# Performance work log

Hardware: AMD Instinct MI355X
Metric: run time of the kernel (lower is better)

The kernel has to match this reference:

```python
import jax, jax.numpy as jnp
import numpy as np

B, C, H, W = 64, 2048, 14, 14
D, S, ITERS, EPS, HID = 256, 8, 3, 1e-8, 512


def build_pos(h, w, d):
    gy, gx = np.meshgrid(np.arange(h), np.arange(w), indexing='ij')
    q = d // 4
    omega = 1.0 / (10000.0 ** (np.arange(q) / q))
    ey = gy.reshape(-1, 1) * omega
    ex = gx.reshape(-1, 1) * omega
    pe = np.concatenate([np.sin(ey), np.cos(ey), np.sin(ex), np.cos(ex)], axis=1)
    return jnp.asarray(pe[None], jnp.float32)  # (1, h*w, d)


def layernorm(x, g, b, eps=1e-5):
    m = x.mean(-1, keepdims=True)
    v = ((x - m) ** 2).mean(-1, keepdims=True)
    return (x - m) * jax.lax.rsqrt(v + eps) * g + b


def setup_inputs() -> dict:
    key = jax.random.key(0)
    ks = jax.random.split(key, 16)
    w = lambda k, shp, s=0.02: jax.random.normal(k, shp, jnp.float32) * s
    inp = {
        'x': jax.random.normal(ks[0], (B, C, H, W), jnp.float32),
        'slot_noise': jax.random.normal(ks[1], (B, S, D), jnp.float32),
        'conv_w': w(ks[2], (C, D)), 'conv_b': jnp.zeros((D,), jnp.float32),
        'pos': build_pos(H, W, D),
        'slots_mu': jax.random.normal(ks[3], (1, 1, D), jnp.float32),
        'slots_logsigma': -jnp.ones((1, 1, D), jnp.float32),
        'qw': w(ks[4], (D, D)), 'qb': jnp.zeros((D,), jnp.float32),
        'kw': w(ks[5], (D, D)), 'kb': jnp.zeros((D,), jnp.float32),
        'vw': w(ks[6], (D, D)), 'vb': jnp.zeros((D,), jnp.float32),
        'gru_wih': w(ks[7], (D, 3 * D)), 'gru_whh': w(ks[8], (D, 3 * D)),
        'gru_bih': jnp.zeros((3 * D,), jnp.float32), 'gru_bhh': jnp.zeros((3 * D,), jnp.float32),
        'w1': w(ks[9], (D, HID)), 'b1': jnp.zeros((HID,), jnp.float32),
        'w2': w(ks[10], (HID, D)), 'b2': jnp.zeros((D,), jnp.float32),
        'ln_in_g': jnp.ones((D,), jnp.float32), 'ln_in_b': jnp.zeros((D,), jnp.float32),
        'ln_s_g': jnp.ones((D,), jnp.float32), 'ln_s_b': jnp.zeros((D,), jnp.float32),
        'ln_ff_g': jnp.ones((D,), jnp.float32), 'ln_ff_b': jnp.zeros((D,), jnp.float32),
    }
    return inp


def reference(x, slot_noise, conv_w, conv_b, pos, slots_mu, slots_logsigma,
              qw, qb, kw, kb, vw, vb, gru_wih, gru_whh, gru_bih, gru_bhh,
              w1, b1, w2, b2, ln_in_g, ln_in_b, ln_s_g, ln_s_b, ln_ff_g, ln_ff_b):
    b, c, h, w_ = x.shape
    d = qw.shape[0]
    scale = d ** (-0.5)
    # (B,C,H,W) -> (B,N,C) -> project -> add pos
    xt = x.transpose(0, 2, 3, 1).reshape(b, h * w_, c)
    xt = xt @ conv_w + conv_b + pos
    # slot init
    slots = slots_mu + jnp.exp(slots_logsigma) * slot_noise  # (B,S,D)
    inp = layernorm(xt, ln_in_g, ln_in_b)
    k = inp @ kw + kb
    v = inp @ vw + vb
    attn = None
    for _ in range(ITERS):
        slots_prev = slots
        s = layernorm(slots, ln_s_g, ln_s_b)
        q = s @ qw + qb
        dots = jnp.einsum('bid,bjd->bij', q, k) * scale  # (B,S,N)
        attn = jax.nn.softmax(dots, axis=1) + EPS  # softmax over slots
        attn = attn / attn.sum(-1, keepdims=True)  # renormalize over keys
        updates = jnp.einsum('bjd,bij->bid', v, attn)  # (B,S,D)
        # GRUCell (torch semantics)
        gi = updates @ gru_wih + gru_bih
        gh = slots_prev @ gru_whh + gru_bhh
        ir, iz, inn = jnp.split(gi, 3, axis=-1)
        hr, hz, hn = jnp.split(gh, 3, axis=-1)
        r = jax.nn.sigmoid(ir + hr)
        z = jax.nn.sigmoid(iz + hz)
        nn_ = jnp.tanh(inn + r * hn)
        slots = (1.0 - z) * nn_ + z * slots_prev
        ff = layernorm(slots, ln_ff_g, ln_ff_b)
        slots = slots + (jax.nn.relu(ff @ w1 + b1)) @ w2 + b2
    attn_map = attn.reshape(b, S, h, w_)
    return slots, attn_map
```

## Files before the change

### kernel.cpp

```cpp
#include <hip/hip_runtime.h>
#include <stdint.h>

#define HWN 196
#define CIN 2048
#define DD  256
#define BB  64
#define NSLOT 8
#define KVPAD 224
#define MTOT 12544
#define BKP 128

typedef __attribute__((ext_vector_type(8))) short short8;
typedef __attribute__((ext_vector_type(4))) float f32x4;
typedef __attribute__((ext_vector_type(4))) unsigned short us4;

__device__ __forceinline__ ushort f2bf(float f){ union{float f;uint32_t u;}v;v.f=f;uint32_t u=v.u;return (ushort)((u+0x7FFFu+((u>>16)&1u))>>16);}
__device__ __forceinline__ float bf2f(ushort h){ union{uint32_t u;float f;}v;v.u=((uint32_t)h)<<16;return v.f;}
__device__ __forceinline__ float sigm(float x){ return 1.f/(1.f+expf(-x)); }

__device__ __forceinline__ short8 ldsY(const ushort* buf, int LD, int kt, int lane){
    int row = lane & 15;
    int ch = kt*4 + (lane>>4);
    return *(const short8*)&buf[row*LD + ((ch ^ (row&7))<<3)];
}
__device__ __forceinline__ short8 gX(const ushort* base, int K, int nrow, int kt, int lane){
    return *(const short8*)&base[(size_t)nrow*K + kt*32 + (lane>>4)*8];
}

struct TD { const float* s; ushort* d; int R, C, t0; };
struct TD8 { TD a[8]; };

__global__ __launch_bounds__(256) void k_prep(TD8 td){
    __shared__ float tile[32][33];
    int bt = blockIdx.x;
    int mi = 0;
    #pragma unroll
    for (int i = 1; i < 8; ++i) if (bt >= td.a[i].t0) mi = i;
    TD d = td.a[mi];
    int lt = bt - d.t0;
    int tilesx = (d.C + 31) >> 5;
    int cb = (lt % tilesx) * 32, rb = (lt / tilesx) * 32;
    int tx = threadIdx.x & 31, ty = threadIdx.x >> 5;
    for (int i = ty; i < 32; i += 8) {
        int r = rb + i, c = cb + tx;
        tile[i][tx] = (r < d.R && c < d.C) ? d.s[(size_t)r * d.C + c] : 0.f;
    }
    __syncthreads();
    for (int i = ty; i < 32; i += 8) {
        int c = cb + i, r = rb + tx;
        if (c < d.C && r < d.R) d.d[(size_t)c * d.R + r] = f2bf(tile[tx][i]);
    }
}

__global__ __launch_bounds__(512) void k_proj(const float* __restrict__ x,
        const ushort* __restrict__ cwT, float* __restrict__ Cpart){
    __shared__ ushort As[2][64*BKP];
    const int t = threadIdx.x, lane = t & 63, wv = t >> 6;
    const int tile = blockIdx.x >> 1, kq = blockIdx.x & 1;
    const int bm = tile * 64;
    const int kbase = kq * 1024;

    const int am = t & 63, kg = t >> 6;
    const int mg = bm + am;
    const int ab = mg / HWN, ap = mg % HWN;
    const float* aptr = x + (size_t)ab*(CIN*HWN) + ap + (size_t)kbase*HWN;

    f32x4 acc[4][2] = {};
    float areg[16];

    #pragma unroll
    for (int j = 0; j < 16; ++j) areg[j] = aptr[(size_t)(kg*16+j)*HWN];
    {
        short8 av0, av1;
        #pragma unroll
        for (int j = 0; j < 8; ++j){ av0[j] = (short)f2bf(areg[j]); av1[j] = (short)f2bf(areg[8+j]); }
        int ch0 = kg*2;
        *(short8*)&As[0][am*BKP + ((ch0^(am&7))<<3)] = av0;
        *(short8*)&As[0][am*BKP + (((ch0+1)^(am&7))<<3)] = av1;
    }
    __syncthreads();
    int cur = 0;
    for (int kt = 0; kt < 8; ++kt){
        if (kt < 7){
            #pragma unroll
            for (int j = 0; j < 16; ++j)
                areg[j] = aptr[(size_t)((kt+1)*BKP + kg*16+j)*HWN];
        }
        short8 bfr[4][2];
        #pragma unroll
        for (int kk = 0; kk < 4; ++kk)
            #pragma unroll
            for (int ni = 0; ni < 2; ++ni){
                int n = wv*32 + ni*16 + (lane&15);
                bfr[kk][ni] = *(const short8*)&cwT[(size_t)n*CIN + kbase + kt*BKP + kk*32 + (lane>>4)*8];
            }
        #pragma unroll
        for (int kk = 0; kk < 4; ++kk){
            short8 afr[4];
            #pragma unroll
            for (int mi = 0; mi < 4; ++mi){
                int row = mi*16 + (lane&15);
                int ch = kk*4 + (lane>>4);
                afr[mi] = *(const short8*)&As[cur][row*BKP + ((ch^(row&7))<<3)];
            }
            #pragma unroll
            for (int mi = 0; mi < 4; ++mi)
                #pragma unroll
                for (int ni = 0; ni < 2; ++ni)
                    acc[mi][ni] = __builtin_amdgcn_mfma_f32_16x16x32_bf16(afr[mi], bfr[kk][ni], acc[mi][ni], 0,0,0);
        }
        if (kt < 7){
            short8 av0, av1;
            #pragma unroll
            for (int j = 0; j < 8; ++j){ av0[j] = (short)f2bf(areg[j]); av1[j] = (short)f2bf(areg[8+j]); }
            int ch0 = kg*2;
            *(short8*)&As[cur^1][am*BKP + ((ch0^(am&7))<<3)] = av0;
            *(short8*)&As[cur^1][am*BKP + (((ch0+1)^(am&7))<<3)] = av1;
        }
        __syncthreads();
        cur ^= 1;
    }
    float* outp = Cpart + (size_t)kq*MTOT*DD;
    #pragma unroll
    for (int mi = 0; mi < 4; ++mi){
        #pragma unroll
        for (int ni = 0; ni < 2; ++ni){
            int n = wv*32 + ni*16 + (lane&15);
            #pragma unroll
            for (int r = 0; r < 4; ++r){
                int m = bm + mi*16 + (lane>>4)*4 + r;
                outp[(size_t)m*DD + n] = acc[mi][ni][r];
            }
        }
    }
}

__global__ __launch_bounds__(512) void k_red(const float* __restrict__ Cpart,
        const float* __restrict__ cb, const float* __restrict__ pos,
        const float* __restrict__ lng, const float* __restrict__ lnb,
        const ushort* __restrict__ kwT, const ushort* __restrict__ vwT,
        const float* __restrict__ kb, const float* __restrict__ vb,
        ushort* __restrict__ kbf, ushort* __restrict__ vT){
    __shared__ ushort As[32*256];
    const int t = threadIdx.x, lane = t & 63, wv = t >> 6;
    const int b = blockIdx.x / 7, pblk = blockIdx.x % 7;
    {
        int row = t >> 4, seg = t & 15;
        int pin = pblk*32 + row;
        int grow = b*HWN + pin;
        if (grow > MTOT-1) grow = MTOT-1;
        int p = pin < HWN ? pin : HWN-1;
        const float* c0 = Cpart + (size_t)grow*DD + seg*16;
        const float* c1 = Cpart + (size_t)MTOT*DD + (size_t)grow*DD + seg*16;
        const float* pp = pos + (size_t)p*DD + seg*16;
        float f[16];
        float s = 0.f, sq = 0.f;
        #pragma unroll
        for (int q = 0; q < 4; ++q){
            f32x4 a  = *(const f32x4*)&c0[q*4];
            f32x4 bq = *(const f32x4*)&c1[q*4];
            f32x4 pv = *(const f32x4*)&pp[q*4];
            f32x4 cv = *(const f32x4*)&cb[seg*16 + q*4];
            #pragma unroll
            for (int r2 = 0; r2 < 4; ++r2){
                float v = a[r2] + bq[r2] + pv[r2] + cv[r2];
                f[q*4+r2] = v; s += v; sq += v*v;
            }
        }
        #pragma unroll
        for (int m = 8; m >= 1; m >>= 1){ s += __shfl_xor(s, m, 64); sq += __shfl_xor(sq, m, 64); }
        float mean = s * (1.f/256.f);
        float rs = rsqrtf(sq*(1.f/256.f) - mean*mean + 1e-5f);
        int d0 = seg*16;
        short8 o0, o1;
        #pragma unroll
        for (int j = 0; j < 8; ++j){
            o0[j] = (short)f2bf((f[j]   - mean)*rs*lng[d0+j]   + lnb[d0+j]);
            o1[j] = (short)f2bf((f[8+j] - mean)*rs*lng[d0+8+j] + lnb[d0+8+j]);
        }
        int ch0 = seg*2;
        *(short8*)&As[row*256 + ((ch0^(row&7))<<3)] = o0;
        *(short8*)&As[row*256 + (((ch0+1)^(row&7))<<3)] = o1;
    }
    __syncthreads();
    f32x4 acck[2][2] = {}, accv[2][2] = {};
    const int n0 = wv*32;
    #pragma unroll
    for (int kt = 0; kt < 8; ++kt){
        short8 afr[2];
        #pragma unroll
        for (int mi = 0; mi < 2; ++mi){
            int row = mi*16 + (lane&15);
            int ch = kt*4 + (lane>>4);
            afr[mi] = *(const short8*)&As[row*256 + ((ch^(row&7))<<3)];
        }
        #pragma unroll
        for (int ni = 0; ni < 2; ++ni){
            int n = n0 + ni*16 + (lane&15);
            int koff = kt*32 + (lane>>4)*8;
            short8 bk = *(const short8*)&kwT[(size_t)n*DD + koff];
            short8 bv = *(const short8*)&vwT[(size_t)n*DD + koff];
            #pragma unroll
            for (int mi = 0; mi < 2; ++mi){
                acck[mi][ni] = __builtin_amdgcn_mfma_f32_16x16x32_bf16(afr[mi], bk, acck[mi][ni],0,0,0);
                accv[mi][ni] = __builtin_amdgcn_mfma_f32_16x16x32_bf16(afr[mi], bv, accv[mi][ni],0,0,0);
            }
        }
    }
    #pragma unroll
    for (int mi = 0; mi < 2; ++mi){
        #pragma unroll
        for (int ni = 0; ni < 2; ++ni){
            int n = n0 + ni*16 + (lane&15);
            float kbn = kb[n], vbn = vb[n];
            int pl0 = pblk*32 + mi*16 + (lane>>4)*4;
            us4 pk;
            #pragma unroll
            for (int r = 0; r < 4; ++r){
                kbf[((size_t)b*KVPAD + pl0 + r)*DD + n] = f2bf(acck[mi][ni][r] + kbn);
                pk[r] = f2bf(accv[mi][ni][r] + vbn);
            }
            *(us4*)&vT[((size_t)b*DD + n)*KVPAD + pl0] = pk;
        }
    }
}

__global__ __launch_bounds__(512) void k_init(const float* __restrict__ noise,
        const float* __restrict__ mu, const float* __restrict__ lsig,
        const ushort* __restrict__ qwT, const float* __restrict__ qb,
        const float* __restrict__ gs, const float* __restrict__ bs,
        float* __restrict__ slots, ushort* __restrict__ qbuf){
    __shared__ float Sld[16*256];
    __shared__ ushort Ysn[16*256];
    __shared__ float part[8][16][2];
    __shared__ float stats[16][2];
    const int t = threadIdx.x, lane = t & 63, w = t >> 6;
    const int bb = blockIdx.x, rbase = bb*16;
    {
        int row = t>>5, ch = t&31; int d = ch*8;
        f32x4 n0 = *(const f32x4*)&noise[(size_t)(rbase+row)*DD + d];
        f32x4 n1 = *(const f32x4*)&noise[(size_t)(rbase+row)*DD + d + 4];
        f32x4 m0 = *(const f32x4*)&mu[d];
        f32x4 m1 = *(const f32x4*)&mu[d+4];
        f32x4 l0 = *(const f32x4*)&lsig[d];
        f32x4 l1 = *(const f32x4*)&lsig[d+4];
        f32x4 s0, s1;
        #pragma unroll
        for (int j = 0; j < 4; ++j){
            s0[j] = m0[j] + expf(l0[j])*n0[j];
            s1[j] = m1[j] + expf(l1[j])*n1[j];
        }
        *(f32x4*)&slots[(size_t)(rbase+row)*DD + d] = s0;
        *(f32x4*)&slots[(size_t)(rbase+row)*DD + d + 4] = s1;
        *(f32x4*)&Sld[row*256 + d] = s0;
        *(f32x4*)&Sld[row*256 + d + 4] = s1;
    }
    __syncthreads();
    f32x4 sv[2];
    #pragma unroll
    for (int sub = 0; sub < 2; ++sub){
        int d0 = w*32 + sub*16 + (lane>>4)*4;
        sv[sub] = *(const f32x4*)&Sld[(lane&15)*256 + d0];
    }
    {
        float lsum = 0.f, lsq = 0.f;
        #pragma unroll
        for (int sub = 0; sub < 2; ++sub)
            #pragma unroll
            for (int r = 0; r < 4; ++r){ float v = sv[sub][r]; lsum += v; lsq += v*v; }
        lsum += __shfl_xor(lsum, 16, 64); lsum += __shfl_xor(lsum, 32, 64);
        lsq  += __shfl_xor(lsq, 16, 64);  lsq  += __shfl_xor(lsq, 32, 64);
        if (lane < 16){ part[w][lane][0] = lsum; part[w][lane][1] = lsq; }
    }
    __syncthreads();
    if (t < 16){
        float a = 0.f, c = 0.f;
        #pragma unroll
        for (int i = 0; i < 8; ++i){ a += part[i][t][0]; c += part[i][t][1]; }
        float mean = a*(1.f/256.f);
        stats[t][0] = mean;
        stats[t][1] = rsqrtf(c*(1.f/256.f) - mean*mean + 1e-5f);
    }
    __syncthreads();
    {
        int slot = lane&15;
        float mean = stats[slot][0], rs = stats[slot][1];
        #pragma unroll
        for (int sub = 0; sub < 2; ++sub){
            int d0 = w*32 + sub*16 + (lane>>4)*4;
            f32x4 g4 = *(const f32x4*)&gs[d0];
            f32x4 b4 = *(const f32x4*)&bs[d0];
            us4 o;
            #pragma unroll
            for (int r = 0; r < 4; ++r) o[r] = f2bf((sv[sub][r]-mean)*rs*g4[r] + b4[r]);
            int ch = d0>>3;
            *(us4*)&Ysn[slot*256 + ((ch^(slot&7))<<3) + (d0&7)] = o;
        }
    }
    __syncthreads();
    f32x4 qa[2] = {};
    #pragma unroll
    for (int kt = 0; kt < 8; ++kt){
        short8 ysn = ldsY(Ysn, 256, kt, lane);
        #pragma unroll
        for (int sub = 0; sub < 2; ++sub){
            int nrow = w*32 + sub*16 + (lane&15);
            short8 xx = gX(qwT, 256, nrow, kt, lane);
            qa[sub] = __builtin_amdgcn_mfma_f32_16x16x32_bf16(xx, ysn, qa[sub], 0,0,0);
        }
    }
    #pragma unroll
    for (int sub = 0; sub < 2; ++sub){
        int qd0 = w*32 + sub*16 + (lane>>4)*4;
        f32x4 qb4 = *(const f32x4*)&qb[qd0];
        us4 o;
        #pragma unroll
        for (int r = 0; r < 4; ++r) o[r] = f2bf((qa[sub][r]+qb4[r])*0.0625f);
        *(us4*)&qbuf[(size_t)(rbase+(lane&15))*DD + qd0] = o;
    }
}

__global__ __launch_bounds__(512) void k_slot(
        const ushort* __restrict__ qbuf, const ushort* __restrict__ kbf,
        const ushort* __restrict__ vT, float* __restrict__ slots,
        ushort* __restrict__ qout,
        const ushort* __restrict__ wihT, const ushort* __restrict__ whhT,
        const float* __restrict__ bih, const float* __restrict__ bhh,
        const ushort* __restrict__ w1T, const float* __restrict__ b1,
        const ushort* __restrict__ w2T, const float* __restrict__ b2,
        const float* __restrict__ gff, const float* __restrict__ bff,
        const float* __restrict__ gs, const float* __restrict__ bs,
        const ushort* __restrict__ qwT, const float* __restrict__ qb,
        float* __restrict__ out_slots, float* __restrict__ out_attn,
        int final_){
    __shared__ ushort Yq[16*256];
    __shared__ ushort Xat[16*256];
    __shared__ ushort Yupd[16*256];
    __shared__ ushort Yslb[16*256];
    __shared__ ushort Ysn[16*256];
    __shared__ ushort Yh[16*512];
    __shared__ float wpart[8][16];
    __shared__ float invk[16];
    __shared__ float part[8][16][2];
    __shared__ float stats[16][2];
    const int t = threadIdx.x, lane = t & 63, w = t >> 6;
    const int b = blockIdx.x;
    const int rbase = b * NSLOT;
    const int srow = lane & 15;
    const int srd = (srow < NSLOT) ? srow : 0;

    if (t < 256){
        int row = t>>5, ch = t&31;
        short8 v = *(const short8*)&qbuf[(size_t)(rbase+row)*DD + ch*8];
        *(short8*)&Yq[row*256 + ((ch^(row&7))<<3)] = v;
        f32x4 s0 = *(const f32x4*)&slots[(size_t)(rbase+row)*DD + ch*8];
        f32x4 s1 = *(const f32x4*)&slots[(size_t)(rbase+row)*DD + ch*8 + 4];
        short8 sv;
        #pragma unroll
        for (int j = 0; j < 4; ++j){ sv[j] = (short)f2bf(s0[j]); sv[4+j] = (short)f2bf(s1[j]); }
        *(short8*)&Yslb[row*256 + ((ch^(row&7))<<3)] = sv;
    } else {
        int i = t - 256;
        int row = (i>>5) + 8, ch = i&31;
        short8 z;
        #pragma unroll
        for (int j = 0; j < 8; ++j) z[j] = 0;
        *(short8*)&Yq[row*256 + ((ch^(row&7))<<3)] = z;
        *(short8*)&Yupd[row*256 + ((ch^(row&7))<<3)] = z;
        *(short8*)&Yslb[row*256 + ((ch^(row&7))<<3)] = z;
    }
    __syncthreads();
    {
        short8 yf[8];
        #pragma unroll
        for (int kt = 0; kt < 8; ++kt) yf[kt] = ldsY(Yq, 256, kt, lane);
        float ps = 0.f;
        #pragma unroll
        for (int rep = 0; rep < 2; ++rep){
            int f = w + rep*8;
            if (f < 14){
                f32x4 acc = {};
                #pragma unroll
                for (int kt = 0; kt < 8; ++kt){
                    short8 xx = gX(kbf + (size_t)b*KVPAD*DD, 256, f*16 + (lane&15), kt, lane);
                    acc = __builtin_amdgcn_mfma_f32_16x16x32_bf16(xx, yf[kt], acc, 0,0,0);
                }
                int k0 = f*16 + (lane>>4)*4;
                us4 o;
                #pragma unroll
                for (int r = 0; r < 4; ++r){
                    float v = acc[r];
                    float mx = v;
                    mx = fmaxf(mx, __shfl_xor(mx, 1, 64));
                    mx = fmaxf(mx, __shfl_xor(mx, 2, 64));
                    mx = fmaxf(mx, __shfl_xor(mx, 4, 64));
                    float e = expf(v - mx);
                    float se = e;
                    se += __shfl_xor(se, 1, 64);
                    se += __shfl_xor(se, 2, 64);
                    se += __shfl_xor(se, 4, 64);
                    float val = e/se + 1e-8f;
                    if (k0 + r >= HWN) val = 0.f;
                    ps += val;
                    o[r] = f2bf(val);
                }
                int ch = k0 >> 3;
                *(us4*)&Xat[srow*256 + ((ch^(srow&7))<<3) + (k0&7)] = o;
            }
        }
        ps += __shfl_xor(ps, 16, 64);
        ps += __shfl_xor(ps, 32, 64);
        if (lane < 16) wpart[w][lane] = ps;
    }
    __syncthreads();
    if (t < 16){
        float s = 0.f;
        #pragma unroll
        for (int i = 0; i < 8; ++i) s += wpart[i][t];
        invk[t] = 1.f/s;
    }
    __syncthreads();
    {
        short8 xa[7];
        #pragma unroll
        for (int kt = 0; kt < 7; ++kt) xa[kt] = ldsY(Xat, 256, kt, lane);
        f32x4 iv = *(const f32x4*)&invk[(lane>>4)*4];
        #pragma unroll
        for (int i = 0; i < 2; ++i){
            int d0 = (w*2 + i)*16;
            f32x4 acc = {};
            #pragma unroll
            for (int kt = 0; kt < 7; ++kt){
                short8 y = gX(vT + (size_t)b*DD*KVPAD, KVPAD, d0 + (lane&15), kt, lane);
                acc = __builtin_amdgcn_mfma_f32_16x16x32_bf16(xa[kt], y, acc, 0,0,0);
            }
            #pragma unroll
            for (int r = 0; r < 4; ++r){
                int s2 = (lane>>4)*4 + r;
                if (s2 < NSLOT){
                    int d = d0 + (lane&15);
                    int ch = d >> 3;
                    Yupd[s2*256 + ((ch^(s2&7))<<3) + (d&7)] = f2bf(acc[r]*iv[r]);
                }
            }
        }
    }
    if (final_){
        for (int idx = t; idx < NSLOT*HWN; idx += 512){
            int slot = idx/HWN, key = idx - slot*HWN;
            int ch = key >> 3;
            out_attn[(size_t)b*NSLOT*HWN + idx] =
                bf2f(Xat[slot*256 + ((ch^(slot&7))<<3) + (key&7)]) * invk[slot];
        }
    }
    __syncthreads();
    f32x4 gi[6] = {}, gh[6] = {};
    #pragma unroll
    for (int kt = 0; kt < 8; ++kt){
        short8 yu = ldsY(Yupd, 256, kt, lane);
        short8 ys = ldsY(Yslb, 256, kt, lane);
        #pragma unroll
        for (int g = 0; g < 3; ++g)
            #pragma unroll
            for (int sub = 0; sub < 2; ++sub){
                int nrow = g*256 + w*32 + sub*16 + (lane&15);
                short8 xi = gX(wihT, 256, nrow, kt, lane);
                short8 xh = gX(whhT, 256, nrow, kt, lane);
                gi[g*2+sub] = __builtin_amdgcn_mfma_f32_16x16x32_bf16(xi, yu, gi[g*2+sub], 0,0,0);
                gh[g*2+sub] = __builtin_amdgcn_mfma_f32_16x16x32_bf16(xh, ys, gh[g*2+sub], 0,0,0);
            }
    }
    f32x4 snew[2];
    #pragma unroll
    for (int sub = 0; sub < 2; ++sub){
        int d0 = w*32 + sub*16 + (lane>>4)*4;
        f32x4 sp  = *(const f32x4*)&slots[(size_t)(rbase + srd)*DD + d0];
        f32x4 bir = *(const f32x4*)&bih[d0];
        f32x4 biz = *(const f32x4*)&bih[256 + d0];
        f32x4 bin = *(const f32x4*)&bih[512 + d0];
        f32x4 bhr = *(const f32x4*)&bhh[d0];
        f32x4 bhz = *(const f32x4*)&bhh[256 + d0];
        f32x4 bhn = *(const f32x4*)&bhh[512 + d0];
        #pragma unroll
        for (int r = 0; r < 4; ++r){
            float ir = gi[0+sub][r] + bir[r];
            float iz = gi[2+sub][r] + biz[r];
            float in_ = gi[4+sub][r] + bin[r];
            float hr = gh[0+sub][r] + bhr[r];
            float hz = gh[2+sub][r] + bhz[r];
            float hn = gh[4+sub][r] + bhn[r];
            float rr = sigm(ir + hr);
            float zz = sigm(iz + hz);
            float nn = tanhf(in_ + rr*hn);
            snew[sub][r] = (1.f - zz)*nn + zz*sp[r];
        }
    }
    {
        float lsum = 0.f, lsq = 0.f;
        #pragma unroll
        for (int sub = 0; sub < 2; ++sub)
            #pragma unroll
            for (int r = 0; r < 4; ++r){ float v = snew[sub][r]; lsum += v; lsq += v*v; }
        lsum += __shfl_xor(lsum, 16, 64); lsum += __shfl_xor(lsum, 32, 64);
        lsq  += __shfl_xor(lsq, 16, 64);  lsq  += __shfl_xor(lsq, 32, 64);
        if (lane < 16){ part[w][lane][0] = lsum; part[w][lane][1] = lsq; }
    }
    __syncthreads();
    if (t < 16){
        float a = 0.f, c = 0.f;
        #pragma unroll
        for (int i = 0; i < 8; ++i){ a += part[i][t][0]; c += part[i][t][1]; }
        float mean = a*(1.f/256.f);
        stats[t][0] = mean;
        stats[t][1] = rsqrtf(c*(1.f/256.f) - mean*mean + 1e-5f);
    }
    __syncthreads();
    {
        float mean = stats[srow][0], rs = stats[srow][1];
        #pragma unroll
        for (int sub = 0; sub < 2; ++sub){
            int d0 = w*32 + sub*16 + (lane>>4)*4;
            f32x4 g4 = *(const f32x4*)&gff[d0];
            f32x4 b4 = *(const f32x4*)&bff[d0];
            us4 o;
            #pragma unroll
            for (int r = 0; r < 4; ++r) o[r] = f2bf((snew[sub][r]-mean)*rs*g4[r] + b4[r]);
            int ch = d0 >> 3;
            *(us4*)&Ysn[srow*256 + ((ch^(srow&7))<<3) + (d0&7)] = o;
        }
    }
    __syncthreads();
    {
        f32x4 hh[4] = {};
        #pragma unroll
        for (int kt = 0; kt < 8; ++kt){
            short8 ysn = ldsY(Ysn, 256, kt, lane);
            #pragma unroll
            for (int s2 = 0; s2 < 4; ++s2){
                int nrow = w*64 + s2*16 + (lane&15);
                short8 xx = gX(w1T, 256, nrow, kt, lane);
                hh[s2] = __builtin_amdgcn_mfma_f32_16x16x32_bf16(xx, ysn, hh[s2], 0,0,0);
            }
        }
        #pragma unroll
        for (int s2 = 0; s2 < 4; ++s2){
            int n0 = w*64 + s2*16 + (lane>>4)*4;
            f32x4 b14 = *(const f32x4*)&b1[n0];
            us4 o;
            #pragma unroll
            for (int r = 0; r < 4; ++r) o[r] = f2bf(fmaxf(hh[s2][r] + b14[r], 0.f));
            int ch = n0 >> 3;
            *(us4*)&Yh[srow*512 + ((ch^(srow&7))<<3) + (n0&7)] = o;
        }
    }
    __syncthreads();
    f32x4 ns[2];
    {
        f32x4 o2[2] = {};
        #pragma unroll
        for (int kt = 0; kt < 16; ++kt){
            short8 yh = ldsY(Yh, 512, kt, lane);
            #pragma unroll
            for (int sub = 0; sub < 2; ++sub){
                int nrow = w*32 + sub*16 + (lane&15);
                short8 xx = gX(w2T, 512, nrow, kt, lane);
                o2[sub] = __builtin_amdgcn_mfma_f32_16x16x32_bf16(xx, yh, o2[sub], 0,0,0);
            }
        }
        float* dst = final_ ? out_slots : slots;
        #pragma unroll
        for (int sub = 0; sub < 2; ++sub){
            int d0 = w*32 + sub*16 + (lane>>4)*4;
            f32x4 b24 = *(const f32x4*)&b2[d0];
            #pragma unroll
            for (int r = 0; r < 4; ++r) ns[sub][r] = o2[sub][r] + b24[r] + snew[sub][r];
            if (srow < NSLOT)
                *(f32x4*)&dst[(size_t)(rbase + srow)*DD + d0] = ns[sub];
        }
    }
    if (final_) return;
    {
        float lsum = 0.f, lsq = 0.f;
        #pragma unroll
        for (int sub = 0; sub < 2; ++sub)
            #pragma unroll
            for (int r = 0; r < 4; ++r){ float v = ns[sub][r]; lsum += v; lsq += v*v; }
        lsum += __shfl_xor(lsum, 16, 64); lsum += __shfl_xor(lsum, 32, 64);
        lsq  += __shfl_xor(lsq, 16, 64);  lsq  += __shfl_xor(lsq, 32, 64);
        if (lane < 16){ part[w][lane][0] = lsum; part[w][lane][1] = lsq; }
    }
    __syncthreads();
    if (t < 16){
        float a = 0.f, c = 0.f;
        #pragma unroll
        for (int i = 0; i < 8; ++i){ a += part[i][t][0]; c += part[i][t][1]; }
        float mean = a*(1.f/256.f);
        stats[t][0] = mean;
        stats[t][1] = rsqrtf(c*(1.f/256.f) - mean*mean + 1e-5f);
    }
    __syncthreads();
    {
        float mean = stats[srow][0], rs = stats[srow][1];
        #pragma unroll
        for (int sub = 0; sub < 2; ++sub){
            int d0 = w*32 + sub*16 + (lane>>4)*4;
            f32x4 g4 = *(const f32x4*)&gs[d0];
            f32x4 b4 = *(const f32x4*)&bs[d0];
            us4 o;
            #pragma unroll
            for (int r = 0; r < 4; ++r) o[r] = f2bf((ns[sub][r]-mean)*rs*g4[r] + b4[r]);
            int ch = d0 >> 3;
            *(us4*)&Ysn[srow*256 + ((ch^(srow&7))<<3) + (d0&7)] = o;
        }
    }
    __syncthreads();
    {
        f32x4 qa[2] = {};
        #pragma unroll
        for (int kt = 0; kt < 8; ++kt){
            short8 ysn = ldsY(Ysn, 256, kt, lane);
            #pragma unroll
            for (int sub = 0; sub < 2; ++sub){
                int nrow = w*32 + sub*16 + (lane&15);
                short8 xx = gX(qwT, 256, nrow, kt, lane);
                qa[sub] = __builtin_amdgcn_mfma_f32_16x16x32_bf16(xx, ysn, qa[sub], 0,0,0);
            }
        }
        #pragma unroll
        for (int sub = 0; sub < 2; ++sub){
            int qd0 = w*32 + sub*16 + (lane>>4)*4;
            f32x4 qb4 = *(const f32x4*)&qb[qd0];
            us4 o;
            #pragma unroll
            for (int r = 0; r < 4; ++r) o[r] = f2bf((qa[sub][r]+qb4[r])*0.0625f);
            if (srow < NSLOT)
                *(us4*)&qout[(size_t)(rbase + srow)*DD + qd0] = o;
        }
    }
}

extern "C" void kernel_launch(void* const* d_in, const int* in_sizes, int n_in,
                              void* d_out, int out_size, void* d_ws, size_t ws_size,
                              hipStream_t stream) {
    const float* x      = (const float*)d_in[0];
    const float* noise  = (const float*)d_in[1];
    const float* conv_w = (const float*)d_in[2];
    const float* conv_b = (const float*)d_in[3];
    const float* pos    = (const float*)d_in[4];
    const float* mu     = (const float*)d_in[5];
    const float* logsig = (const float*)d_in[6];
    const float* qw  = (const float*)d_in[7];
    const float* qb  = (const float*)d_in[8];
    const float* kw  = (const float*)d_in[9];
    const float* kb  = (const float*)d_in[10];
    const float* vw  = (const float*)d_in[11];
    const float* vb  = (const float*)d_in[12];
    const float* wih = (const float*)d_in[13];
    const float* whh = (const float*)d_in[14];
    const float* bih = (const float*)d_in[15];
    const float* bhh = (const float*)d_in[16];
    const float* w1  = (const float*)d_in[17];
    const float* b1  = (const float*)d_in[18];
    const float* w2  = (const float*)d_in[19];
    const float* b2  = (const float*)d_in[20];
    const float* g_in = (const float*)d_in[21];
    const float* b_in = (const float*)d_in[22];
    const float* g_s  = (const float*)d_in[23];
    const float* b_s  = (const float*)d_in[24];
    const float* g_ff = (const float*)d_in[25];
    const float* b_ff = (const float*)d_in[26];

    char* w = (char*)d_ws;
    ushort* kbf    = (ushort*)w; w += (size_t)BB*KVPAD*DD*2;
    ushort* vT     = (ushort*)w; w += (size_t)BB*DD*KVPAD*2;
    ushort* cwT    = (ushort*)w; w += (size_t)DD*CIN*2;
    ushort* qwT    = (ushort*)w; w += (size_t)DD*DD*2;
    ushort* kwT    = (ushort*)w; w += (size_t)DD*DD*2;
    ushort* vwT    = (ushort*)w; w += (size_t)DD*DD*2;
    ushort* wihT   = (ushort*)w; w += (size_t)768*DD*2;
    ushort* whhT   = (ushort*)w; w += (size_t)768*DD*2;
    ushort* w1T    = (ushort*)w; w += (size_t)512*DD*2;
    ushort* w2T    = (ushort*)w; w += (size_t)DD*512*2;
    ushort* qbb    = (ushort*)w; w += (size_t)BB*NSLOT*DD*2;
    float*  slotsb = (float*)w;  w += (size_t)BB*NSLOT*DD*4;
    float*  Cpart  = (float*)w;  w += (size_t)2*MTOT*DD*4;

    float* out_slots = (float*)d_out;
    float* out_attn  = (float*)d_out + (size_t)BB*NSLOT*DD;

    TD8 td;
    td.a[0] = { conv_w, cwT, 2048, 256,    0 };
    td.a[1] = { qw,     qwT,  256, 256,  512 };
    td.a[2] = { kw,     kwT,  256, 256,  576 };
    td.a[3] = { vw,     vwT,  256, 256,  640 };
    td.a[4] = { wih,    wihT, 256, 768,  704 };
    td.a[5] = { whh,    whhT, 256, 768,  896 };
    td.a[6] = { w1,     w1T,  256, 512, 1088 };
    td.a[7] = { w2,     w2T,  512, 256, 1216 };

    k_prep<<<1344, 256, 0, stream>>>(td);
    k_proj<<<392, 512, 0, stream>>>(x, cwT, Cpart);
    k_red<<<448, 512, 0, stream>>>(Cpart, conv_b, pos, g_in, b_in,
                                   kwT, vwT, kb, vb, kbf, vT);
    k_init<<<32, 512, 0, stream>>>(noise, mu, logsig, qwT, qb, g_s, b_s, slotsb, qbb);
    for (int it = 0; it < 3; ++it){
        k_slot<<<BB, 512, 0, stream>>>(qbb, kbf, vT, slotsb, qbb,
                                       wihT, whhT, bih, bhh, w1T, b1, w2T, b2,
                                       g_ff, b_ff, g_s, b_s, qwT, qb,
                                       out_slots, out_attn, it == 2);
    }
}
```

Baseline: 241.2 us.

## Widen split-K in projection and double slot-kernel threads with prefetched weights

The projection GEMM now splits K four ways when workspace allows, giving 784 blocks instead of 392, and the reduce kernel sums a variable number of partials. The slot-iteration kernel goes from 512 to 1024 threads, so each wave owns one 16-column tile, and all weight fragment loads are double-buffered from global memory. This targets the poor GPU fill from only 64 slot blocks and the 392-block projection, at the cost of extra partial-sum traffic and more per-block barrier overhead.

```diff
diff --git a/kernel.cpp b/kernel.cpp
--- a/kernel.cpp
+++ b/kernel.cpp
@@ -53,12 +53,13 @@
 }
 
 __global__ __launch_bounds__(512) void k_proj(const float* __restrict__ x,
-        const ushort* __restrict__ cwT, float* __restrict__ Cpart){
+        const ushort* __restrict__ cwT, float* __restrict__ Cpart,
+        int SK, int ksteps){
     __shared__ ushort As[2][64*BKP];
     const int t = threadIdx.x, lane = t & 63, wv = t >> 6;
-    const int tile = blockIdx.x >> 1, kq = blockIdx.x & 1;
+    const int tile = blockIdx.x / SK, kq = blockIdx.x % SK;
     const int bm = tile * 64;
-    const int kbase = kq * 1024;
+    const int kbase = kq * (ksteps * BKP);
 
     const int am = t & 63, kg = t >> 6;
     const int mg = bm + am;
@@ -80,8 +81,8 @@
     }
     __syncthreads();
     int cur = 0;
-    for (int kt = 0; kt < 8; ++kt){
-        if (kt < 7){
+    for (int kt = 0; kt < ksteps; ++kt){
+        if (kt < ksteps-1){
             #pragma unroll
             for (int j = 0; j < 16; ++j)
                 areg[j] = aptr[(size_t)((kt+1)*BKP + kg*16+j)*HWN];
@@ -109,7 +110,7 @@
                 for (int ni = 0; ni < 2; ++ni)
                     acc[mi][ni] = __builtin_amdgcn_mfma_f32_16x16x32_bf16(afr[mi], bfr[kk][ni], acc[mi][ni], 0,0,0);
         }
-        if (kt < 7){
+        if (kt < ksteps-1){
             short8 av0, av1;
             #pragma unroll
             for (int j = 0; j < 8; ++j){ av0[j] = (short)f2bf(areg[j]); av1[j] = (short)f2bf(areg[8+j]); }
@@ -135,7 +136,7 @@
     }
 }
 
-__global__ __launch_bounds__(512) void k_red(const float* __restrict__ Cpart,
+__global__ __launch_bounds__(512) void k_red(const float* __restrict__ Cpart, int SK,
         const float* __restrict__ cb, const float* __restrict__ pos,
         const float* __restrict__ lng, const float* __restrict__ lnb,
         const ushort* __restrict__ kwT, const ushort* __restrict__ vwT,
@@ -150,23 +151,27 @@
         int grow = b*HWN + pin;
         if (grow > MTOT-1) grow = MTOT-1;
         int p = pin < HWN ? pin : HWN-1;
-        const float* c0 = Cpart + (size_t)grow*DD + seg*16;
-        const float* c1 = Cpart + (size_t)MTOT*DD + (size_t)grow*DD + seg*16;
         const float* pp = pos + (size_t)p*DD + seg*16;
         float f[16];
-        float s = 0.f, sq = 0.f;
         #pragma unroll
         for (int q = 0; q < 4; ++q){
-            f32x4 a  = *(const f32x4*)&c0[q*4];
-            f32x4 bq = *(const f32x4*)&c1[q*4];
             f32x4 pv = *(const f32x4*)&pp[q*4];
             f32x4 cv = *(const f32x4*)&cb[seg*16 + q*4];
             #pragma unroll
-            for (int r2 = 0; r2 < 4; ++r2){
-                float v = a[r2] + bq[r2] + pv[r2] + cv[r2];
-                f[q*4+r2] = v; s += v; sq += v*v;
-            }
-        }
+            for (int r2 = 0; r2 < 4; ++r2) f[q*4+r2] = pv[r2] + cv[r2];
+        }
+        for (int sk = 0; sk < SK; ++sk){
+            const float* cp = Cpart + (size_t)sk*MTOT*DD + (size_t)grow*DD + seg*16;
+            #pragma unroll
+            for (int q = 0; q < 4; ++q){
+                f32x4 a = *(const f32x4*)&cp[q*4];
+                #pragma unroll
+                for (int r2 = 0; r2 < 4; ++r2) f[q*4+r2] += a[r2];
+            }
+        }
+        float s = 0.f, sq = 0.f;
+        #pragma unroll
+        for (int j = 0; j < 16; ++j){ s += f[j]; sq += f[j]*f[j]; }
         #pragma unroll
         for (int m = 8; m >= 1; m >>= 1){ s += __shfl_xor(s, m, 64); sq += __shfl_xor(sq, m, 64); }
         float mean = s * (1.f/256.f);
@@ -320,7 +325,33 @@
     }
 }
 
-__global__ __launch_bounds__(512) void k_slot(
+__device__ __forceinline__ float sm_ep(f32x4 acc, int f, int lane, ushort* Xat, int srow){
+    int k0 = f*16 + (lane>>4)*4;
+    us4 o;
+    float ps = 0.f;
+    #pragma unroll
+    for (int r = 0; r < 4; ++r){
+        float v = acc[r];
+        float mx = v;
+        mx = fmaxf(mx, __shfl_xor(mx, 1, 64));
+        mx = fmaxf(mx, __shfl_xor(mx, 2, 64));
+        mx = fmaxf(mx, __shfl_xor(mx, 4, 64));
+        float e = expf(v - mx);
+        float se = e;
+        se += __shfl_xor(se, 1, 64);
+        se += __shfl_xor(se, 2, 64);
+        se += __shfl_xor(se, 4, 64);
+        float val = e/se + 1e-8f;
+        if (k0 + r >= HWN) val = 0.f;
+        ps += val;
+        o[r] = f2bf(val);
+    }
+    int ch = k0 >> 3;
+    *(us4*)&Xat[srow*256 + ((ch^(srow&7))<<3) + (k0&7)] = o;
+    return ps;
+}
+
+__global__ __launch_bounds__(1024, 4) void k_slot(
         const ushort* __restrict__ qbuf, const ushort* __restrict__ kbf,
         const ushort* __restrict__ vT, float* __restrict__ slots,
         ushort* __restrict__ qout,
@@ -339,9 +370,9 @@
     __shared__ ushort Yslb[16*256];
     __shared__ ushort Ysn[16*256];
     __shared__ ushort Yh[16*512];
-    __shared__ float wpart[8][16];
+    __shared__ float wpart[16][16];
     __shared__ float invk[16];
-    __shared__ float part[8][16][2];
+    __shared__ float part[16][16][2];
     __shared__ float stats[16][2];
     const int t = threadIdx.x, lane = t & 63, w = t >> 6;
     const int b = blockIdx.x;
@@ -359,7 +390,7 @@
         #pragma unroll
         for (int j = 0; j < 4; ++j){ sv[j] = (short)f2bf(s0[j]); sv[4+j] = (short)f2bf(s1[j]); }
         *(short8*)&Yslb[row*256 + ((ch^(row&7))<<3)] = sv;
-    } else {
+    } else if (t < 512){
         int i = t - 256;
         int row = (i>>5) + 8, ch = i&31;
         short8 z;
@@ -370,83 +401,69 @@
         *(short8*)&Yslb[row*256 + ((ch^(row&7))<<3)] = z;
     }
     __syncthreads();
-    {
+    if (w < 14){
         short8 yf[8];
         #pragma unroll
         for (int kt = 0; kt < 8; ++kt) yf[kt] = ldsY(Yq, 256, kt, lane);
-        float ps = 0.f;
-        #pragma unroll
-        for (int rep = 0; rep < 2; ++rep){
-            int f = w + rep*8;
-            if (f < 14){
-                f32x4 acc = {};
-                #pragma unroll
-                for (int kt = 0; kt < 8; ++kt){
-                    short8 xx = gX(kbf + (size_t)b*KVPAD*DD, 256, f*16 + (lane&15), kt, lane);
-                    acc = __builtin_amdgcn_mfma_f32_16x16x32_bf16(xx, yf[kt], acc, 0,0,0);
-                }
-                int k0 = f*16 + (lane>>4)*4;
-                us4 o;
-                #pragma unroll
-                for (int r = 0; r < 4; ++r){
-                    float v = acc[r];
-                    float mx = v;
-                    mx = fmaxf(mx, __shfl_xor(mx, 1, 64));
-                    mx = fmaxf(mx, __shfl_xor(mx, 2, 64));
-                    mx = fmaxf(mx, __shfl_xor(mx, 4, 64));
-                    float e = expf(v - mx);
-                    float se = e;
-                    se += __shfl_xor(se, 1, 64);
-                    se += __shfl_xor(se, 2, 64);
-                    se += __shfl_xor(se, 4, 64);
-                    float val = e/se + 1e-8f;
-                    if (k0 + r >= HWN) val = 0.f;
-                    ps += val;
-                    o[r] = f2bf(val);
-                }
-                int ch = k0 >> 3;
-                *(us4*)&Xat[srow*256 + ((ch^(srow&7))<<3) + (k0&7)] = o;
-            }
-        }
+        const ushort* kb_ = kbf + (size_t)b*KVPAD*DD;
+        const int r0 = w*16 + (lane&15);
+        short8 xa[2];
+        xa[0] = gX(kb_, 256, r0, 0, lane);
+        f32x4 accA = {};
+        #pragma unroll
+        for (int kt = 0; kt < 8; ++kt){
+            int cu = kt & 1, nx = cu ^ 1;
+            if (kt < 7) xa[nx] = gX(kb_, 256, r0, kt+1, lane);
+            accA = __builtin_amdgcn_mfma_f32_16x16x32_bf16(xa[cu], yf[kt], accA, 0,0,0);
+        }
+        float ps = sm_ep(accA, w, lane, Xat, srow);
         ps += __shfl_xor(ps, 16, 64);
         ps += __shfl_xor(ps, 32, 64);
         if (lane < 16) wpart[w][lane] = ps;
+    } else {
+        if (lane < 16) wpart[w][lane] = 0.f;
     }
     __syncthreads();
     if (t < 16){
         float s = 0.f;
         #pragma unroll
-        for (int i = 0; i < 8; ++i) s += wpart[i][t];
+        for (int i = 0; i < 16; ++i) s += wpart[i][t];
         invk[t] = 1.f/s;
     }
-    __syncthreads();
-    {
-        short8 xa[7];
-        #pragma unroll
-        for (int kt = 0; kt < 7; ++kt) xa[kt] = ldsY(Xat, 256, kt, lane);
+    f32x4 pv;
+    {
+        short8 xat[7];
+        #pragma unroll
+        for (int kt = 0; kt < 7; ++kt) xat[kt] = ldsY(Xat, 256, kt, lane);
+        const ushort* vb_ = vT + (size_t)b*DD*KVPAD;
+        const int d0r = w*16 + (lane&15);
+        short8 ya[2];
+        ya[0] = gX(vb_, KVPAD, d0r, 0, lane);
+        f32x4 aA = {};
+        #pragma unroll
+        for (int kt = 0; kt < 7; ++kt){
+            int cu = kt & 1, nx = cu ^ 1;
+            if (kt < 6) ya[nx] = gX(vb_, KVPAD, d0r, kt+1, lane);
+            aA = __builtin_amdgcn_mfma_f32_16x16x32_bf16(xat[kt], ya[cu], aA, 0,0,0);
+        }
+        pv = aA;
+    }
+    __syncthreads();
+    {
         f32x4 iv = *(const f32x4*)&invk[(lane>>4)*4];
-        #pragma unroll
-        for (int i = 0; i < 2; ++i){
-            int d0 = (w*2 + i)*16;
-            f32x4 acc = {};
-            #pragma unroll
-            for (int kt = 0; kt < 7; ++kt){
-                short8 y = gX(vT + (size_t)b*DD*KVPAD, KVPAD, d0 + (lane&15), kt, lane);
-                acc = __builtin_amdgcn_mfma_f32_16x16x32_bf16(xa[kt], y, acc, 0,0,0);
-            }
-            #pragma unroll
-            for (int r = 0; r < 4; ++r){
-                int s2 = (lane>>4)*4 + r;
-                if (s2 < NSLOT){
-                    int d = d0 + (lane&15);
-                    int ch = d >> 3;
-                    Yupd[s2*256 + ((ch^(s2&7))<<3) + (d&7)] = f2bf(acc[r]*iv[r]);
-                }
+        int d0 = w*16;
+        #pragma unroll
+        for (int r = 0; r < 4; ++r){
+            int s2 = (lane>>4)*4 + r;
+            if (s2 < NSLOT){
+                int d = d0 + (lane&15);
+                int ch = d >> 3;
+                Yupd[s2*256 + ((ch^(s2&7))<<3) + (d&7)] = f2bf(pv[r]*iv[r]);
             }
         }
     }
     if (final_){
-        for (int idx = t; idx < NSLOT*HWN; idx += 512){
+        for (int idx = t; idx < NSLOT*HWN; idx += 1024){
             int slot = idx/HWN, key = idx - slot*HWN;
             int ch = key >> 3;
             out_attn[(size_t)b*NSLOT*HWN + idx] =
@@ -454,26 +471,39 @@
         }
     }
     __syncthreads();
-    f32x4 gi[6] = {}, gh[6] = {};
-    #pragma unroll
-    for (int kt = 0; kt < 8; ++kt){
-        short8 yu = ldsY(Yupd, 256, kt, lane);
-        short8 ys = ldsY(Yslb, 256, kt, lane);
-        #pragma unroll
-        for (int g = 0; g < 3; ++g)
-            #pragma unroll
-            for (int sub = 0; sub < 2; ++sub){
-                int nrow = g*256 + w*32 + sub*16 + (lane&15);
-                short8 xi = gX(wihT, 256, nrow, kt, lane);
-                short8 xh = gX(whhT, 256, nrow, kt, lane);
-                gi[g*2+sub] = __builtin_amdgcn_mfma_f32_16x16x32_bf16(xi, yu, gi[g*2+sub], 0,0,0);
-                gh[g*2+sub] = __builtin_amdgcn_mfma_f32_16x16x32_bf16(xh, ys, gh[g*2+sub], 0,0,0);
-            }
-    }
-    f32x4 snew[2];
-    #pragma unroll
-    for (int sub = 0; sub < 2; ++sub){
-        int d0 = w*32 + sub*16 + (lane>>4)*4;
+    f32x4 gi[3] = {}, gh[3] = {};
+    {
+        int nrw[3];
+        #pragma unroll
+        for (int g = 0; g < 3; ++g) nrw[g] = g*256 + w*16 + (lane&15);
+        short8 xw[2][6];
+        #pragma unroll
+        for (int g = 0; g < 3; ++g){
+            xw[0][g]   = gX(wihT, 256, nrw[g], 0, lane);
+            xw[0][3+g] = gX(whhT, 256, nrw[g], 0, lane);
+        }
+        #pragma unroll
+        for (int kt = 0; kt < 8; ++kt){
+            int cu = kt & 1, nx = cu ^ 1;
+            if (kt < 7){
+                #pragma unroll
+                for (int g = 0; g < 3; ++g){
+                    xw[nx][g]   = gX(wihT, 256, nrw[g], kt+1, lane);
+                    xw[nx][3+g] = gX(whhT, 256, nrw[g], kt+1, lane);
+                }
+            }
+            short8 yu = ldsY(Yupd, 256, kt, lane);
+            short8 ys = ldsY(Yslb, 256, kt, lane);
+            #pragma unroll
+            for (int g = 0; g < 3; ++g){
+                gi[g] = __builtin_amdgcn_mfma_f32_16x16x32_bf16(xw[cu][g],   yu, gi[g], 0,0,0);
+                gh[g] = __builtin_amdgcn_mfma_f32_16x16x32_bf16(xw[cu][3+g], ys, gh[g], 0,0,0);
+            }
+        }
+    }
+    f32x4 snew;
+    {
+        int d0 = w*16 + (lane>>4)*4;
         f32x4 sp  = *(const f32x4*)&slots[(size_t)(rbase + srd)*DD + d0];
         f32x4 bir = *(const f32x4*)&bih[d0];
         f32x4 biz = *(const f32x4*)&bih[256 + d0];
@@ -483,24 +513,22 @@
         f32x4 bhn = *(const f32x4*)&bhh[512 + d0];
         #pragma unroll
         for (int r = 0; r < 4; ++r){
-            float ir = gi[0+sub][r] + bir[r];
-            float iz = gi[2+sub][r] + biz[r];
-            float in_ = gi[4+sub][r] + bin[r];
-            float hr = gh[0+sub][r] + bhr[r];
-            float hz = gh[2+sub][r] + bhz[r];
-            float hn = gh[4+sub][r] + bhn[r];
+            float ir = gi[0][r] + bir[r];
+            float iz = gi[1][r] + biz[r];
+            float in_ = gi[2][r] + bin[r];
+            float hr = gh[0][r] + bhr[r];
+            float hz = gh[1][r] + bhz[r];
+            float hn = gh[2][r] + bhn[r];
             float rr = sigm(ir + hr);
             float zz = sigm(iz + hz);
             float nn = tanhf(in_ + rr*hn);
-            snew[sub][r] = (1.f - zz)*nn + zz*sp[r];
+            snew[r] = (1.f - zz)*nn + zz*sp[r];
         }
     }
     {
         float lsum = 0.f, lsq = 0.f;
         #pragma unroll
-        for (int sub = 0; sub < 2; ++sub)
-            #pragma unroll
-            for (int r = 0; r < 4; ++r){ float v = snew[sub][r]; lsum += v; lsq += v*v; }
+        for (int r = 0; r < 4; ++r){ float v = snew[r]; lsum += v; lsq += v*v; }
         lsum += __shfl_xor(lsum, 16, 64); lsum += __shfl_xor(lsum, 32, 64);
         lsq  += __shfl_xor(lsq, 16, 64);  lsq  += __shfl_xor(lsq, 32, 64);
         if (lane < 16){ part[w][lane][0] = lsum; part[w][lane][1] = lsq; }
@@ -509,7 +537,7 @@
     if (t < 16){
         float a = 0.f, c = 0.f;
         #pragma unroll
-        for (int i = 0; i < 8; ++i){ a += part[i][t][0]; c += part[i][t][1]; }
+        for (int i = 0; i < 16; ++i){ a += part[i][t][0]; c += part[i][t][1]; }
         float mean = a*(1.f/256.f);
         stats[t][0] = mean;
         stats[t][1] = rsqrtf(c*(1.f/256.f) - mean*mean + 1e-5f);
@@ -517,34 +545,39 @@
     __syncthreads();
     {
         float mean = stats[srow][0], rs = stats[srow][1];
-        #pragma unroll
-        for (int sub = 0; sub < 2; ++sub){
-            int d0 = w*32 + sub*16 + (lane>>4)*4;
-            f32x4 g4 = *(const f32x4*)&gff[d0];
-            f32x4 b4 = *(const f32x4*)&bff[d0];
-            us4 o;
-            #pragma unroll
-            for (int r = 0; r < 4; ++r) o[r] = f2bf((snew[sub][r]-mean)*rs*g4[r] + b4[r]);
-            int ch = d0 >> 3;
-            *(us4*)&Ysn[srow*256 + ((ch^(srow&7))<<3) + (d0&7)] = o;
-        }
-    }
-    __syncthreads();
-    {
-        f32x4 hh[4] = {};
+        int d0 = w*16 + (lane>>4)*4;
+        f32x4 g4 = *(const f32x4*)&gff[d0];
+        f32x4 b4 = *(const f32x4*)&bff[d0];
+        us4 o;
+        #pragma unroll
+        for (int r = 0; r < 4; ++r) o[r] = f2bf((snew[r]-mean)*rs*g4[r] + b4[r]);
+        int ch = d0 >> 3;
+        *(us4*)&Ysn[srow*256 + ((ch^(srow&7))<<3) + (d0&7)] = o;
+    }
+    __syncthreads();
+    {
+        int nr1[2];
+        #pragma unroll
+        for (int s2 = 0; s2 < 2; ++s2) nr1[s2] = w*32 + s2*16 + (lane&15);
+        short8 xw1[2][2];
+        #pragma unroll
+        for (int s2 = 0; s2 < 2; ++s2) xw1[0][s2] = gX(w1T, 256, nr1[s2], 0, lane);
+        f32x4 hh[2] = {};
         #pragma unroll
         for (int kt = 0; kt < 8; ++kt){
+            int cu = kt & 1, nx = cu ^ 1;
+            if (kt < 7){
+                #pragma unroll
+                for (int s2 = 0; s2 < 2; ++s2) xw1[nx][s2] = gX(w1T, 256, nr1[s2], kt+1, lane);
+            }
             short8 ysn = ldsY(Ysn, 256, kt, lane);
             #pragma unroll
-            for (int s2 = 0; s2 < 4; ++s2){
-                int nrow = w*64 + s2*16 + (lane&15);
-                short8 xx = gX(w1T, 256, nrow, kt, lane);
-                hh[s2] = __builtin_amdgcn_mfma_f32_16x16x32_bf16(xx, ysn, hh[s2], 0,0,0);
-            }
-        }
-        #pragma unroll
-        for (int s2 = 0; s2 < 4; ++s2){
-            int n0 = w*64 + s2*16 + (lane>>4)*4;
+            for (int s2 = 0; s2 < 2; ++s2)
+                hh[s2] = __builtin_amdgcn_mfma_f32_16x16x32_bf16(xw1[cu][s2], ysn, hh[s2], 0,0,0);
+        }
+        #pragma unroll
+        for (int s2 = 0; s2 < 2; ++s2){
+            int n0 = w*32 + s2*16 + (lane>>4)*4;
             f32x4 b14 = *(const f32x4*)&b1[n0];
             us4 o;
             #pragma unroll
@@ -554,37 +587,32 @@
         }
     }
     __syncthreads();
-    f32x4 ns[2];
-    {
-        f32x4 o2[2] = {};
+    f32x4 ns;
+    {
+        int nr2 = w*16 + (lane&15);
+        short8 xw2[2];
+        xw2[0] = gX(w2T, 512, nr2, 0, lane);
+        f32x4 o2 = {};
         #pragma unroll
         for (int kt = 0; kt < 16; ++kt){
+            int cu = kt & 1, nx = cu ^ 1;
+            if (kt < 15) xw2[nx] = gX(w2T, 512, nr2, kt+1, lane);
             short8 yh = ldsY(Yh, 512, kt, lane);
-            #pragma unroll
-            for (int sub = 0; sub < 2; ++sub){
-                int nrow = w*32 + sub*16 + (lane&15);
-                short8 xx = gX(w2T, 512, nrow, kt, lane);
-                o2[sub] = __builtin_amdgcn_mfma_f32_16x16x32_bf16(xx, yh, o2[sub], 0,0,0);
-            }
+            o2 = __builtin_amdgcn_mfma_f32_16x16x32_bf16(xw2[cu], yh, o2, 0,0,0);
         }
         float* dst = final_ ? out_slots : slots;
-        #pragma unroll
-        for (int sub = 0; sub < 2; ++sub){
-            int d0 = w*32 + sub*16 + (lane>>4)*4;
-            f32x4 b24 = *(const f32x4*)&b2[d0];
-            #pragma unroll
-            for (int r = 0; r < 4; ++r) ns[sub][r] = o2[sub][r] + b24[r] + snew[sub][r];
-            if (srow < NSLOT)
-                *(f32x4*)&dst[(size_t)(rbase + srow)*DD + d0] = ns[sub];
-        }
+        int d0 = w*16 + (lane>>4)*4;
+        f32x4 b24 = *(const f32x4*)&b2[d0];
+        #pragma unroll
+        for (int r = 0; r < 4; ++r) ns[r] = o2[r] + b24[r] + snew[r];
+        if (srow < NSLOT)
+            *(f32x4*)&dst[(size_t)(rbase + srow)*DD + d0] = ns;
     }
     if (final_) return;
     {
         float lsum = 0.f, lsq = 0.f;
         #pragma unroll
-        for (int sub = 0; sub < 2; ++sub)
-            #pragma unroll
-            for (int r = 0; r < 4; ++r){ float v = ns[sub][r]; lsum += v; lsq += v*v; }
+        for (int r = 0; r < 4; ++r){ float v = ns[r]; lsum += v; lsq += v*v; }
         lsum += __shfl_xor(lsum, 16, 64); lsum += __shfl_xor(lsum, 32, 64);
         lsq  += __shfl_xor(lsq, 16, 64);  lsq  += __shfl_xor(lsq, 32, 64);
         if (lane < 16){ part[w][lane][0] = lsum; part[w][lane][1] = lsq; }
@@ -593,7 +621,7 @@
     if (t < 16){
         float a = 0.f, c = 0.f;
         #pragma unroll
-        for (int i = 0; i < 8; ++i){ a += part[i][t][0]; c += part[i][t][1]; }
+        for (int i = 0; i < 16; ++i){ a += part[i][t][0]; c += part[i][t][1]; }
         float mean = a*(1.f/256.f);
         stats[t][0] = mean;
         stats[t][1] = rsqrtf(c*(1.f/256.f) - mean*mean + 1e-5f);
@@ -601,41 +629,35 @@
     __syncthreads();
     {
         float mean = stats[srow][0], rs = stats[srow][1];
-        #pragma unroll
-        for (int sub = 0; sub < 2; ++sub){
-            int d0 = w*32 + sub*16 + (lane>>4)*4;
-            f32x4 g4 = *(const f32x4*)&gs[d0];
-            f32x4 b4 = *(const f32x4*)&bs[d0];
-            us4 o;
-            #pragma unroll
-            for (int r = 0; r < 4; ++r) o[r] = f2bf((ns[sub][r]-mean)*rs*g4[r] + b4[r]);
-            int ch = d0 >> 3;
-            *(us4*)&Ysn[srow*256 + ((ch^(srow&7))<<3) + (d0&7)] = o;
-        }
-    }
-    __syncthreads();
-    {
-        f32x4 qa[2] = {};
+        int d0 = w*16 + (lane>>4)*4;
+        f32x4 g4 = *(const f32x4*)&gs[d0];
+        f32x4 b4 = *(const f32x4*)&bs[d0];
+        us4 o;
+        #pragma unroll
+        for (int r = 0; r < 4; ++r) o[r] = f2bf((ns[r]-mean)*rs*g4[r] + b4[r]);
+        int ch = d0 >> 3;
+        *(us4*)&Ysn[srow*256 + ((ch^(srow&7))<<3) + (d0&7)] = o;
+    }
+    __syncthreads();
+    {
+        int nrq = w*16 + (lane&15);
+        short8 xq[2];
+        xq[0] = gX(qwT, 256, nrq, 0, lane);
+        f32x4 qa = {};
         #pragma unroll
         for (int kt = 0; kt < 8; ++kt){
+            int cu = kt & 1, nx = cu ^ 1;
+            if (kt < 7) xq[nx] = gX(qwT, 256, nrq, kt+1, lane);
             short8 ysn = ldsY(Ysn, 256, kt, lane);
-            #pragma unroll
-            for (int sub = 0; sub < 2; ++sub){
-                int nrow = w*32 + sub*16 + (lane&15);
-                short8 xx = gX(qwT, 256, nrow, kt, lane);
-                qa[sub] = __builtin_amdgcn_mfma_f32_16x16x32_bf16(xx, ysn, qa[sub], 0,0,0);
-            }
-        }
-        #pragma unroll
-        for (int sub = 0; sub < 2; ++sub){
-            int qd0 = w*32 + sub*16 + (lane>>4)*4;
-            f32x4 qb4 = *(const f32x4*)&qb[qd0];
-            us4 o;
-            #pragma unroll
-            for (int r = 0; r < 4; ++r) o[r] = f2bf((qa[sub][r]+qb4[r])*0.0625f);
-            if (srow < NSLOT)
-                *(us4*)&qout[(size_t)(rbase + srow)*DD + qd0] = o;
-        }
+            qa = __builtin_amdgcn_mfma_f32_16x16x32_bf16(xq[cu], ysn, qa, 0,0,0);
+        }
+        int qd0 = w*16 + (lane>>4)*4;
+        f32x4 qb4 = *(const f32x4*)&qb[qd0];
+        us4 o;
+        #pragma unroll
+        for (int r = 0; r < 4; ++r) o[r] = f2bf((qa[r]+qb4[r])*0.0625f);
+        if (srow < NSLOT)
+            *(us4*)&qout[(size_t)(rbase + srow)*DD + qd0] = o;
     }
 }
 
@@ -683,7 +705,10 @@
     ushort* w2T    = (ushort*)w; w += (size_t)DD*512*2;
     ushort* qbb    = (ushort*)w; w += (size_t)BB*NSLOT*DD*2;
     float*  slotsb = (float*)w;  w += (size_t)BB*NSLOT*DD*4;
-    float*  Cpart  = (float*)w;  w += (size_t)2*MTOT*DD*4;
+    float*  Cpart  = (float*)w;
+    size_t fixedBytes = (size_t)(w - (char*)d_ws);
+    int SK = (fixedBytes + (size_t)4*MTOT*DD*4 <= ws_size) ? 4 : 2;
+    int ksteps = 16 / SK;
 
     float* out_slots = (float*)d_out;
     float* out_attn  = (float*)d_out + (size_t)BB*NSLOT*DD;
@@ -699,14 +724,14 @@
     td.a[7] = { w2,     w2T,  512, 256, 1216 };
 
     k_prep<<<1344, 256, 0, stream>>>(td);
-    k_proj<<<392, 512, 0, stream>>>(x, cwT, Cpart);
-    k_red<<<448, 512, 0, stream>>>(Cpart, conv_b, pos, g_in, b_in,
+    k_proj<<<196*SK, 512, 0, stream>>>(x, cwT, Cpart, SK, ksteps);
+    k_red<<<448, 512, 0, stream>>>(Cpart, SK, conv_b, pos, g_in, b_in,
                                    kwT, vwT, kb, vb, kbf, vT);
     k_init<<<32, 512, 0, stream>>>(noise, mu, logsig, qwT, qb, g_s, b_s, slotsb, qbb);
     for (int it = 0; it < 3; ++it){
-        k_slot<<<BB, 512, 0, stream>>>(qbb, kbf, vT, slotsb, qbb,
-                                       wihT, whhT, bih, bhh, w1T, b1, w2T, b2,
-                                       g_ff, b_ff, g_s, b_s, qwT, qb,
-                                       out_slots, out_attn, it == 2);
-    }
-}
+        k_slot<<<BB, 1024, 0, stream>>>(qbb, kbf, vT, slotsb, qbb,
+                                        wihT, whhT, bih, bhh, w1T, b1, w2T, b2,
+                                        g_ff, b_ff, g_s, b_s, qwT, qb,
+                                        out_slots, out_attn, it == 2);
+    }
+}
```

Result: no change. 243.5 us (+0.9%).
